# Kernel tuning notes

Measured on AMD Instinct MI355X. Metric: run time of the kernel, lower is better.

Reference implementation:

```python
import jax, jax.numpy as jnp
import numpy as np

N, E, D = 20000, 320000, 512


def _gat(x, W, a_src, a_dst, bias, src, dst, n, heads, ch):
    # PyG GATConv (eval mode, add_self_loops already applied via src/dst)
    h = (x @ W).reshape(n, heads, ch)              # [n, H, C]
    es = (h * a_src).sum(-1)                       # [n, H]
    ed = (h * a_dst).sum(-1)                       # [n, H]
    e = jax.nn.leaky_relu(es[src] + ed[dst], 0.2)  # [E, H]
    # edge-softmax grouped by destination node
    m = jax.ops.segment_max(e, dst, num_segments=n)
    ex = jnp.exp(e - m[dst])
    z = jax.ops.segment_sum(ex, dst, num_segments=n)
    alpha = ex / (z[dst] + 1e-16)                  # [E, H]
    out = jax.ops.segment_sum(h[src] * alpha[:, :, None], dst, num_segments=n)
    return out.reshape(n, heads * ch) + bias


def _ln(x, g, b):
    mu = x.mean(-1, keepdims=True)
    v = ((x - mu) ** 2).mean(-1, keepdims=True)
    return (x - mu) * jax.lax.rsqrt(v + 1e-5) * g + b


def setup_inputs() -> dict:
    key = jax.random.key(0)
    ks = jax.random.split(key, 24)
    p = lambda k, shape: jax.random.normal(k, shape, dtype=jnp.float32) * 0.05
    inp = {
        'x': jax.random.normal(ks[0], (N, D), dtype=jnp.float32),
        'edge_index': jax.random.randint(ks[1], (2, E), 0, N, dtype=jnp.int32),
        # GAT layer 1: 512 -> 8 heads x 128
        'w1': p(ks[2], (D, 1024)), 'as1': p(ks[3], (8, 128)), 'ad1': p(ks[4], (8, 128)), 'b1': jnp.zeros((1024,), jnp.float32),
        'g1': jnp.ones((1024,), jnp.float32), 'be1': jnp.zeros((1024,), jnp.float32),
        # GAT layer 2: 1024 -> 4 heads x 64
        'w2': p(ks[5], (1024, 256)), 'as2': p(ks[6], (4, 64)), 'ad2': p(ks[7], (4, 64)), 'b2': jnp.zeros((256,), jnp.float32),
        'g2': jnp.ones((256,), jnp.float32), 'be2': jnp.zeros((256,), jnp.float32),
        # GAT layer 3: 256 -> 2 heads x 32
        'w3': p(ks[8], (256, 64)), 'as3': p(ks[9], (2, 32)), 'ad3': p(ks[10], (2, 32)), 'b3': jnp.zeros((64,), jnp.float32),
        'g3': jnp.ones((64,), jnp.float32), 'be3': jnp.zeros((64,), jnp.float32),
        # anomaly scorer MLP
        'sw1': p(ks[11], (64, 64)), 'sb1': jnp.zeros((64,), jnp.float32),
        'sg1': jnp.ones((64,), jnp.float32), 'sbe1': jnp.zeros((64,), jnp.float32),
        'sw2': p(ks[12], (64, 32)), 'sb2': jnp.zeros((32,), jnp.float32),
        'sg2': jnp.ones((32,), jnp.float32), 'sbe2': jnp.zeros((32,), jnp.float32),
        'sw3': p(ks[13], (32, 1)), 'sb3': jnp.zeros((1,), jnp.float32),
    }
    return inp


def reference(x, edge_index, w1, as1, ad1, b1, g1, be1,
              w2, as2, ad2, b2, g2, be2,
              w3, as3, ad3, b3, g3, be3,
              sw1, sb1, sg1, sbe1, sw2, sb2, sg2, sbe2, sw3, sb3):
    loops = jnp.arange(N, dtype=edge_index.dtype)
    src = jnp.concatenate([edge_index[0], loops])  # add self-loops (PyG default)
    dst = jnp.concatenate([edge_index[1], loops])

    h1 = jax.nn.relu(_gat(x, w1, as1, ad1, b1, src, dst, N, 8, 128))
    h1 = _ln(h1, g1, be1)
    h2 = jax.nn.relu(_gat(h1, w2, as2, ad2, b2, src, dst, N, 4, 64))
    h2 = _ln(h2, g2, be2)
    h2 = h2 + h1[:, :256]
    h3 = jax.nn.relu(_gat(h2, w3, as3, ad3, b3, src, dst, N, 2, 32))
    h3 = _ln(h3, g3, be3)
    h3 = h3 + h2[:, :64]

    s = jax.nn.relu(h3 @ sw1 + sb1)
    s = _ln(s, sg1, sbe1)
    s = jax.nn.relu(s @ sw2 + sb2)
    s = _ln(s, sg2, sbe2)
    return jax.nn.sigmoid(s @ sw3 + sb3)  # [N, 1]
```

## Files before the change

### kernel.cpp

```cpp
#include <hip/hip_runtime.h>
#include <hip/hip_bf16.h>
#include <hip/hip_fp16.h>
#include <cstdint>

#define NN 20000
#define EE 320000
#define ETOT (EE + NN)

using f32x4 = __attribute__((ext_vector_type(4))) float;
using f16x8 = __attribute__((ext_vector_type(8))) _Float16;
typedef unsigned short ushortT;

__global__ void hist_kernel(const int* __restrict__ ei, int* __restrict__ deg) {
  int i = blockIdx.x * 256 + threadIdx.x;
  if (i >= ETOT) return;
  int d = (i < EE) ? ei[EE + i] : (i - EE);
  atomicAdd(&deg[d], 1);
}

__global__ __launch_bounds__(1024) void scan_kernel(const int* __restrict__ deg,
                                                    int* __restrict__ row_ptr,
                                                    int* __restrict__ cursor) {
  __shared__ int partial[1024];
  const int t = threadIdx.x;
  constexpr int PER = (NN + 1023) / 1024;
  const int base = t * PER;
  int vals[PER];
  int local = 0;
  #pragma unroll
  for (int j = 0; j < PER; ++j) {
    int i = base + j;
    int v = (i < NN) ? deg[i] : 0;
    vals[j] = v; local += v;
  }
  partial[t] = local;
  __syncthreads();
  for (int off = 1; off < 1024; off <<= 1) {
    int x = (t >= off) ? partial[t - off] : 0;
    __syncthreads();
    partial[t] += x;
    __syncthreads();
  }
  int prefix = partial[t] - local;
  #pragma unroll
  for (int j = 0; j < PER; ++j) {
    int i = base + j;
    if (i < NN) { row_ptr[i] = prefix; cursor[i] = prefix; }
    prefix += vals[j];
  }
  if (t == 1023) row_ptr[NN] = prefix;
}

__global__ void scatter_kernel(const int* __restrict__ ei, int* __restrict__ cursor,
                               int* __restrict__ csr_src) {
  int i = blockIdx.x * 256 + threadIdx.x;
  if (i >= ETOT) return;
  int s, d;
  if (i < EE) { s = ei[i]; d = ei[EE + i]; } else { s = d = i - EE; }
  int pos = atomicAdd(&cursor[d], 1);
  csr_src[pos] = s;
}

__global__ void half_mat(const float* __restrict__ a, __half* __restrict__ o, int n) {
  int i = blockIdx.x * 256 + threadIdx.x;
  if (i >= n) return;
  o[i] = __float2half(a[i]);
}

__global__ void tsplit_f16(const float* __restrict__ w, ushortT* __restrict__ hi,
                           ushortT* __restrict__ lo, int K, int M) {
  int i = blockIdx.x * 256 + threadIdx.x;
  if (i >= K * M) return;
  int k = i / M, c = i - k * M;
  float v = w[i];
  __half h = __float2half(v);
  __half l = __float2half(v - __half2float(h));
  size_t o = (size_t)c * K + k;
  hi[o] = __half_as_ushort(h);
  lo[o] = __half_as_ushort(l);
}

__device__ __forceinline__ void gload16(const void* g, void* l) {
  __builtin_amdgcn_global_load_lds((const __attribute__((address_space(1))) void*)g,
                                   (__attribute__((address_space(3))) void*)l, 16, 0, 0);
}

template<int BM, int BN, int FM, int FN, int CHEAD>
__global__ __launch_bounds__(256) void gemm_f16(
    const __half* __restrict__ A,
    const ushortT* __restrict__ Bhi, const ushortT* __restrict__ Blo,
    __half* __restrict__ C, int M, int Ncols, int K,
    const float* __restrict__ asrc, const float* __restrict__ adst,
    float* __restrict__ es_g, float* __restrict__ ed_g, int H)
{
  constexpr int BK = 32;
  __shared__ ushortT lds[(BM + 2 * BN) * BK];
  ushortT* sA  = lds;
  ushortT* sBh = sA + BM * BK;
  ushortT* sBl = sBh + BN * BK;

  const int tid  = threadIdx.x;
  const int lane = tid & 63;
  const int wid  = tid >> 6;
  const int wm   = (wid >> 1) * (FM * 16);
  const int wn   = (wid & 1) * (FN * 16);
  const int row0 = blockIdx.x * BM;
  const int col0 = blockIdx.y * BN;
  const int r    = lane & 15;
  const int kg   = lane >> 4;

  const ushortT* Au = (const ushortT*)A;
  f32x4 acc[FM][FN] = {};

  for (int k0 = 0; k0 < K; k0 += BK) {
    #pragma unroll
    for (int i = tid; i < BM * 4; i += 256) {
      int row = i >> 2, slot = i & 3;
      int gs = slot ^ (row & 3);
      int grow = row0 + row; if (grow > M - 1) grow = M - 1;
      gload16(Au + (size_t)grow * K + k0 + gs * 8, sA + row * BK + slot * 8);
    }
    #pragma unroll
    for (int i = tid; i < BN * 4; i += 256) {
      int row = i >> 2, slot = i & 3;
      int gs = slot ^ (row & 3);
      size_t go = (size_t)(col0 + row) * K + k0 + gs * 8;
      gload16(Bhi + go, sBh + row * BK + slot * 8);
      gload16(Blo + go, sBl + row * BK + slot * 8);
    }
    __syncthreads();

    const int ks = (kg ^ (r & 3)) * 8;
    f16x8 a[FM], bh[FN], bl[FN];
    #pragma unroll
    for (int mi = 0; mi < FM; ++mi)
      a[mi] = *(const f16x8*)(sA + (wm + mi * 16 + r) * BK + ks);
    #pragma unroll
    for (int ni = 0; ni < FN; ++ni) {
      int off = (wn + ni * 16 + r) * BK + ks;
      bh[ni] = *(const f16x8*)(sBh + off);
      bl[ni] = *(const f16x8*)(sBl + off);
    }
    #pragma unroll
    for (int mi = 0; mi < FM; ++mi)
      #pragma unroll
      for (int ni = 0; ni < FN; ++ni) {
        acc[mi][ni] = __builtin_amdgcn_mfma_f32_16x16x32_f16(a[mi], bh[ni], acc[mi][ni], 0, 0, 0);
        acc[mi][ni] = __builtin_amdgcn_mfma_f32_16x16x32_f16(a[mi], bl[ni], acc[mi][ni], 0, 0, 0);
      }
    __syncthreads();
  }

  #pragma unroll
  for (int mi = 0; mi < FM; ++mi) {
    int rb = row0 + wm + mi * 16 + (lane >> 4) * 4;
    #pragma unroll
    for (int ni = 0; ni < FN; ++ni) {
      int cc = col0 + wn + ni * 16 + (lane & 15);
      #pragma unroll
      for (int j = 0; j < 4; ++j) {
        int rr = rb + j;
        if (rr < M) C[(size_t)rr * Ncols + cc] = __float2half(acc[mi][ni][j]);
      }
    }
  }

  constexpr bool DIRECT = (CHEAD == FN * 16);
  float av[FN], dv[FN];
  #pragma unroll
  for (int ni = 0; ni < FN; ++ni) {
    int cc = col0 + wn + ni * 16 + (lane & 15);
    av[ni] = asrc[cc];
    dv[ni] = adst[cc];
  }
  float ps[FM][4], pd[FM][4];
  #pragma unroll
  for (int mi = 0; mi < FM; ++mi)
    #pragma unroll
    for (int j = 0; j < 4; ++j) {
      float s = 0.f, d = 0.f;
      #pragma unroll
      for (int ni = 0; ni < FN; ++ni) {
        float v = acc[mi][ni][j];
        s += v * av[ni];
        d += v * dv[ni];
      }
      #pragma unroll
      for (int off = 8; off; off >>= 1) {
        s += __shfl_xor(s, off);
        d += __shfl_xor(d, off);
      }
      ps[mi][j] = s; pd[mi][j] = d;
    }
  const int head = (col0 + wn) / CHEAD;
  if constexpr (DIRECT) {
    if ((lane & 15) == 0) {
      #pragma unroll
      for (int mi = 0; mi < FM; ++mi)
        #pragma unroll
        for (int j = 0; j < 4; ++j) {
          int rr = row0 + wm + mi * 16 + (lane >> 4) * 4 + j;
          if (rr < M) { es_g[rr * H + head] = ps[mi][j]; ed_g[rr * H + head] = pd[mi][j]; }
        }
    }
  } else {
    float* l_es = (float*)lds;
    float* l_ed = l_es + BM;
    if ((wid & 1) == 0 && (lane & 15) == 0) {
      #pragma unroll
      for (int mi = 0; mi < FM; ++mi)
        #pragma unroll
        for (int j = 0; j < 4; ++j) {
          int rl = wm + mi * 16 + (lane >> 4) * 4 + j;
          l_es[rl] = ps[mi][j]; l_ed[rl] = pd[mi][j];
        }
    }
    __syncthreads();
    if ((wid & 1) == 1 && (lane & 15) == 0) {
      #pragma unroll
      for (int mi = 0; mi < FM; ++mi)
        #pragma unroll
        for (int j = 0; j < 4; ++j) {
          int rl = wm + mi * 16 + (lane >> 4) * 4 + j;
          int rr = row0 + rl;
          if (rr < M) {
            es_g[rr * H + head] = ps[mi][j] + l_es[rl];
            ed_g[rr * H + head] = pd[mi][j] + l_ed[rl];
          }
        }
    }
  }
}

template<int VPT> struct GVec;
template<> struct GVec<16> { uint4 a, b; };
template<> struct GVec<4>  { uint2 a; };
template<> struct GVec<1>  { ushortT a; };

template<int VPT>
__device__ __forceinline__ GVec<VPT> gload(const __half* p) {
  GVec<VPT> v;
  if constexpr (VPT == 16) { v.a = *(const uint4*)p; v.b = *(const uint4*)(p + 8); }
  else if constexpr (VPT == 4) { v.a = *(const uint2*)p; }
  else { v.a = *(const ushortT*)p; }
  return v;
}

template<int VPT>
__device__ __forceinline__ void gfma(const GVec<VPT>& u, float w, float* acc) {
  if constexpr (VPT == 1) {
    __half hv;
    *(ushortT*)&hv = u.a;
    acc[0] += w * __half2float(hv);
  } else {
    const __half2* p = (const __half2*)&u;
    #pragma unroll
    for (int j = 0; j < VPT / 2; ++j) {
      float2 f = __half22float2(p[j]);
      acc[2 * j]     += w * f.x;
      acc[2 * j + 1] += w * f.y;
    }
  }
}

template<int H, int C, bool RES_IN, bool F16_OUT, bool SCORER, int WPB>
__global__ __launch_bounds__(WPB * 64, 2) void gat_agg_wave(
    const __half* __restrict__ h, const float* __restrict__ es_g, const float* __restrict__ ed_g,
    const int* __restrict__ row_ptr, const int* __restrict__ csr_src,
    const float* __restrict__ bias, const float* __restrict__ gamma, const float* __restrict__ beta,
    const __half* __restrict__ res_in, int res_stride, __half* __restrict__ out_h,
    const float* __restrict__ sw1, const float* __restrict__ sb1,
    const float* __restrict__ sg1, const float* __restrict__ sbe1,
    const float* __restrict__ sw2, const float* __restrict__ sb2,
    const float* __restrict__ sg2, const float* __restrict__ sbe2,
    const float* __restrict__ sw3, const float* __restrict__ sb3,
    float* __restrict__ out)
{
  constexpr int HC   = H * C;
  constexpr int VPT  = HC / 64;
  constexpr int CH   = 32;
  constexpr int BB   = (VPT == 16) ? 4 : 8;
  constexpr int LOGH = (H == 8) ? 3 : ((H == 4) ? 2 : 1);
  constexpr int EPR  = 64 >> LOGH;
  constexpr int ROUNDS = CH / EPR;

  const int wave = threadIdx.x >> 6;
  const int lane = threadIdx.x & 63;
  const int n    = blockIdx.x * WPB + wave;
  const int c0   = lane * VPT;
  const int myh  = c0 / C;
  const int wh   = lane & (H - 1);

  __shared__ float w_lds[WPB][(CH * H < 64) ? 64 : CH * H];
  float* wl = w_lds[wave];

  const int p0 = row_ptr[n];
  const int p1 = row_ptr[n + 1];
  const float edw = ed_g[n * H + wh];

  float acc[VPT];
  #pragma unroll
  for (int j = 0; j < VPT; ++j) acc[j] = 0.f;
  float z = 0.f;

  for (int base = p0; base < p1; base += CH) {
    const int m = min(CH, p1 - base);
    int sv = n;
    if (lane < CH) {
      int idx = base + lane;
      if (idx < p1) sv = csr_src[idx];
    }
    #pragma unroll
    for (int r = 0; r < ROUNDS; ++r) {
      int e = (lane >> LOGH) + r * EPR;
      int s = __shfl(sv, e);
      float w = 0.f;
      if (base + e < p1) {
        float ev = es_g[s * H + wh] + edw;
        ev = (ev >= 0.f) ? ev : 0.2f * ev;
        w = __expf(ev);
      }
      wl[e * H + wh] = w;
    }

    const int nb = m / BB;
    GVec<VPT> uA[BB], uB[BB];
    float wA[BB], wB[BB];

    auto LOADB = [&](int b, GVec<VPT> (&u)[BB], float (&w)[BB]) {
      #pragma unroll
      for (int k = 0; k < BB; ++k) {
        int e = b * BB + k;
        int s = __shfl(sv, e);
        w[k] = wl[e * H + myh];
        u[k] = gload<VPT>(h + (size_t)s * HC + c0);
      }
    };
    auto FMAB = [&](GVec<VPT> (&u)[BB], float (&w)[BB]) {
      #pragma unroll
      for (int k = 0; k < BB; ++k) {
        z += w[k];
        gfma<VPT>(u[k], w[k], acc);
      }
    };

    if (nb > 0) LOADB(0, uA, wA);
    #pragma unroll
    for (int bb = 0; bb < CH / BB; bb += 2) {
      if (bb < nb) {
        if (bb + 1 < nb) LOADB(bb + 1, uB, wB);
        FMAB(uA, wA);
      }
      if (bb + 1 < nb) {
        if (bb + 2 < nb) LOADB(bb + 2, uA, wA);
        FMAB(uB, wB);
      }
    }
    for (int e = nb * BB; e < m; ++e) {
      int s = __shfl(sv, e);
      float w = wl[e * H + myh];
      z += w;
      GVec<VPT> u = gload<VPT>(h + (size_t)s * HC + c0);
      gfma<VPT>(u, w, acc);
    }
  }

  float inv = 1.f / (z + 1e-16f);
  float ov[VPT];
  float psum = 0.f, psq = 0.f;
  #pragma unroll
  for (int j = 0; j < VPT; ++j) {
    float x = fmaxf(acc[j] * inv + bias[c0 + j], 0.f);
    ov[j] = x; psum += x; psq += x * x;
  }
  #pragma unroll
  for (int o = 32; o > 0; o >>= 1) {
    psum += __shfl_xor(psum, o);
    psq  += __shfl_xor(psq, o);
  }
  float mu  = psum / (float)HC;
  float var = psq / (float)HC - mu * mu;
  float rs  = rsqrtf(var + 1e-5f);

  ushortT hb[VPT > 1 ? VPT : 2];
  #pragma unroll
  for (int j = 0; j < VPT; ++j) {
    int c = c0 + j;
    float o = (ov[j] - mu) * rs * gamma[c] + beta[c];
    if constexpr (RES_IN) o += __half2float(res_in[(size_t)n * res_stride + c]);
    ov[j] = o;
    if constexpr (F16_OUT) hb[j] = __half_as_ushort(__float2half(o));
  }
  if constexpr (F16_OUT) {
    ushortT* po = (ushortT*)out_h + (size_t)n * HC + c0;
    if constexpr (VPT == 16) {
      *(uint4*)po       = *(uint4*)&hb[0];
      *(uint4*)(po + 8) = *(uint4*)&hb[8];
    } else if constexpr (VPT == 4) {
      *(uint2*)po = *(uint2*)&hb[0];
    } else {
      *po = hb[0];
    }
  }

  if constexpr (SCORER) {
    wl[lane] = ov[0];
    float s1 = sb1[lane];
    #pragma unroll 16
    for (int k = 0; k < 64; ++k) s1 += wl[k] * sw1[k * 64 + lane];
    s1 = fmaxf(s1, 0.f);
    float su = s1, sq = s1 * s1;
    #pragma unroll
    for (int o = 32; o > 0; o >>= 1) { su += __shfl_xor(su, o); sq += __shfl_xor(sq, o); }
    float mu1 = su * (1.f / 64.f), var1 = sq * (1.f / 64.f) - mu1 * mu1;
    float v1 = (s1 - mu1) * rsqrtf(var1 + 1e-5f) * sg1[lane] + sbe1[lane];
    wl[lane] = v1;
    float o2 = 0.f;
    if (lane < 32) {
      o2 = sb2[lane];
      #pragma unroll 16
      for (int k = 0; k < 64; ++k) o2 += wl[k] * sw2[k * 32 + lane];
      o2 = fmaxf(o2, 0.f);
    }
    float su2 = o2, sq2 = o2 * o2;
    #pragma unroll
    for (int o = 16; o > 0; o >>= 1) { su2 += __shfl_xor(su2, o); sq2 += __shfl_xor(sq2, o); }
    float p = 0.f;
    if (lane < 32) {
      float mu2 = su2 * (1.f / 32.f), var2 = sq2 * (1.f / 32.f) - mu2 * mu2;
      float v2 = (o2 - mu2) * rsqrtf(var2 + 1e-5f) * sg2[lane] + sbe2[lane];
      p = v2 * sw3[lane];
    }
    #pragma unroll
    for (int o = 16; o > 0; o >>= 1) p += __shfl_xor(p, o);
    if (lane == 0) out[n] = 1.f / (1.f + expf(-(p + sb3[0])));
  }
}

extern "C" void kernel_launch(void* const* d_in, const int* in_sizes, int n_in,
                              void* d_out, int out_size, void* d_ws, size_t ws_size,
                              hipStream_t stream)
{
  const float* x    = (const float*)d_in[0];
  const int*   ei   = (const int*)d_in[1];
  const float* w1   = (const float*)d_in[2];
  const float* as1  = (const float*)d_in[3];
  const float* ad1  = (const float*)d_in[4];
  const float* b1   = (const float*)d_in[5];
  const float* g1v  = (const float*)d_in[6];
  const float* be1  = (const float*)d_in[7];
  const float* w2   = (const float*)d_in[8];
  const float* as2  = (const float*)d_in[9];
  const float* ad2  = (const float*)d_in[10];
  const float* b2   = (const float*)d_in[11];
  const float* g2v  = (const float*)d_in[12];
  const float* be2  = (const float*)d_in[13];
  const float* w3   = (const float*)d_in[14];
  const float* as3  = (const float*)d_in[15];
  const float* ad3  = (const float*)d_in[16];
  const float* b3   = (const float*)d_in[17];
  const float* g3v  = (const float*)d_in[18];
  const float* be3  = (const float*)d_in[19];
  const float* sw1  = (const float*)d_in[20];
  const float* sb1  = (const float*)d_in[21];
  const float* sg1  = (const float*)d_in[22];
  const float* sbe1 = (const float*)d_in[23];
  const float* sw2  = (const float*)d_in[24];
  const float* sb2  = (const float*)d_in[25];
  const float* sg2  = (const float*)d_in[26];
  const float* sbe2 = (const float*)d_in[27];
  const float* sw3  = (const float*)d_in[28];
  const float* sb3  = (const float*)d_in[29];
  float* out = (float*)d_out;

  char* ws = (char*)d_ws;
  size_t off = 0;
  auto alloc = [&](size_t bytes) -> void* {
    off = (off + 255) & ~(size_t)255;
    void* p = ws + off;
    off += bytes;
    return p;
  };

  __half*  h_gemm  = (__half*)alloc((size_t)NN * 1024 * 2);
  __half*  h1_f16  = (__half*)alloc((size_t)NN * 1024 * 2);
  __half*  h2_f16  = (__half*)alloc((size_t)NN * 256 * 2);
  __half*  x16     = (__half*)alloc((size_t)NN * 512 * 2);
  ushortT* w1t_hi  = (ushortT*)alloc((size_t)512 * 1024 * 2);
  ushortT* w1t_lo  = (ushortT*)alloc((size_t)512 * 1024 * 2);
  ushortT* w2t_hi  = (ushortT*)alloc((size_t)1024 * 256 * 2);
  ushortT* w2t_lo  = (ushortT*)alloc((size_t)1024 * 256 * 2);
  ushortT* w3t_hi  = (ushortT*)alloc((size_t)256 * 64 * 2);
  ushortT* w3t_lo  = (ushortT*)alloc((size_t)256 * 64 * 2);
  float*   es_buf  = (float*)alloc((size_t)NN * 8 * 4);
  float*   ed_buf  = (float*)alloc((size_t)NN * 8 * 4);
  int*     deg     = (int*)alloc((size_t)NN * 4);
  int*     row_ptr = (int*)alloc((size_t)(NN + 1) * 4);
  int*     cursor  = (int*)alloc((size_t)NN * 4);
  int*     csr_src = (int*)alloc((size_t)ETOT * 4);
  (void)ws_size; (void)in_sizes; (void)n_in; (void)out_size;

  hipMemsetAsync(deg, 0, (size_t)NN * 4, stream);
  hist_kernel<<<(ETOT + 255) / 256, 256, 0, stream>>>(ei, deg);
  scan_kernel<<<1, 1024, 0, stream>>>(deg, row_ptr, cursor);
  scatter_kernel<<<(ETOT + 255) / 256, 256, 0, stream>>>(ei, cursor, csr_src);

  half_mat<<<(NN * 512 + 255) / 256, 256, 0, stream>>>(x, x16, NN * 512);
  tsplit_f16<<<(512 * 1024 + 255) / 256, 256, 0, stream>>>(w1, w1t_hi, w1t_lo, 512, 1024);
  tsplit_f16<<<(1024 * 256 + 255) / 256, 256, 0, stream>>>(w2, w2t_hi, w2t_lo, 1024, 256);
  tsplit_f16<<<(256 * 64 + 255) / 256, 256, 0, stream>>>(w3, w3t_hi, w3t_lo, 256, 64);

  const int MB = (NN + 127) / 128;

  gemm_f16<128, 128, 4, 4, 128><<<dim3(MB, 1024 / 128), 256, 0, stream>>>(
      x16, w1t_hi, w1t_lo, h_gemm, NN, 1024, 512, as1, ad1, es_buf, ed_buf, 8);
  gat_agg_wave<8, 128, false, true, false, 4><<<NN / 4, 256, 0, stream>>>(
      h_gemm, es_buf, ed_buf, row_ptr, csr_src, b1, g1v, be1,
      nullptr, 0, h1_f16,
      nullptr, nullptr, nullptr, nullptr, nullptr, nullptr, nullptr, nullptr, nullptr, nullptr, nullptr);

  gemm_f16<128, 128, 4, 4, 64><<<dim3(MB, 256 / 128), 256, 0, stream>>>(
      h1_f16, w2t_hi, w2t_lo, h_gemm, NN, 256, 1024, as2, ad2, es_buf, ed_buf, 4);
  gat_agg_wave<4, 64, true, true, false, 4><<<NN / 4, 256, 0, stream>>>(
      h_gemm, es_buf, ed_buf, row_ptr, csr_src, b2, g2v, be2,
      h1_f16, 1024, h2_f16,
      nullptr, nullptr, nullptr, nullptr, nullptr, nullptr, nullptr, nullptr, nullptr, nullptr, nullptr);

  gemm_f16<128, 64, 4, 2, 32><<<dim3(MB, 1), 256, 0, stream>>>(
      h2_f16, w3t_hi, w3t_lo, h_gemm, NN, 64, 256, as3, ad3, es_buf, ed_buf, 2);
  gat_agg_wave<2, 32, true, false, true, 4><<<NN / 4, 256, 0, stream>>>(
      h_gemm, es_buf, ed_buf, row_ptr, csr_src, b3, g3v, be3,
      h2_f16, 256, nullptr,
      sw1, sb1, sg1, sbe1, sw2, sb2, sg2, sbe2, sw3, sb3, out);
}
```

Baseline: 382.8 us.

## Double-buffer GEMM LDS stages and vectorize GAT aggregation index/weight loads

The GEMM now double-buffers its LDS tiles. It issues the next K-tile's global-to-LDS loads before computing on the current one, using explicit vmcnt waits and raw barriers in place of __syncthreads, so load latency overlaps the MFMA work. In the aggregation kernel, source indices are staged in LDS instead of being broadcast with per-edge shuffles. Attention weights are stored head-major with padding so four weights and four indices can be read as float4/int4. The batch size BB is fixed at 4 for every layer. This doubles GEMM LDS use, which may reduce occupancy, and relies on the hand-coded vmcnt counts matching the number of issued loads.

```diff
diff --git a/kernel.cpp b/kernel.cpp
--- a/kernel.cpp
+++ b/kernel.cpp
@@ -85,6 +85,13 @@
                                    (__attribute__((address_space(3))) void*)l, 16, 0, 0);
 }
 
+template<int N> __device__ __forceinline__ void wait_vm() {
+  if constexpr (N == 0) asm volatile("s_waitcnt vmcnt(0)" ::: "memory");
+  else if constexpr (N == 4) asm volatile("s_waitcnt vmcnt(4)" ::: "memory");
+  else if constexpr (N == 6) asm volatile("s_waitcnt vmcnt(6)" ::: "memory");
+  else static_assert(N == 0 || N == 4 || N == 6, "unsupported vmcnt");
+}
+
 template<int BM, int BN, int FM, int FN, int CHEAD>
 __global__ __launch_bounds__(256) void gemm_f16(
     const __half* __restrict__ A,
@@ -93,11 +100,10 @@
     const float* __restrict__ asrc, const float* __restrict__ adst,
     float* __restrict__ es_g, float* __restrict__ ed_g, int H)
 {
-  constexpr int BK = 32;
-  __shared__ ushortT lds[(BM + 2 * BN) * BK];
-  ushortT* sA  = lds;
-  ushortT* sBh = sA + BM * BK;
-  ushortT* sBl = sBh + BN * BK;
+  constexpr int BK   = 32;
+  constexpr int HALF = (BM + 2 * BN) * BK;
+  constexpr int NL   = (BM * 4 + BN * 8) / 256;
+  __shared__ ushortT lds[2 * HALF];
 
   const int tid  = threadIdx.x;
   const int lane = tid & 63;
@@ -110,9 +116,11 @@
   const int kg   = lane >> 4;
 
   const ushortT* Au = (const ushortT*)A;
-  f32x4 acc[FM][FN] = {};
-
-  for (int k0 = 0; k0 < K; k0 += BK) {
+
+  auto STAGE = [&](int buf, int k0) {
+    ushortT* sA  = lds + buf * HALF;
+    ushortT* sBh = sA + BM * BK;
+    ushortT* sBl = sBh + BN * BK;
     #pragma unroll
     for (int i = tid; i < BM * 4; i += 256) {
       int row = i >> 2, slot = i & 3;
@@ -128,8 +136,21 @@
       gload16(Bhi + go, sBh + row * BK + slot * 8);
       gload16(Blo + go, sBl + row * BK + slot * 8);
     }
-    __syncthreads();
-
+  };
+
+  f32x4 acc[FM][FN] = {};
+  const int nt = K / BK;
+
+  STAGE(0, 0);
+  for (int t = 0; t < nt; ++t) {
+    if (t + 1 < nt) { STAGE((t + 1) & 1, (t + 1) * BK); wait_vm<NL>(); }
+    else            { wait_vm<0>(); }
+    __builtin_amdgcn_s_barrier();
+    __builtin_amdgcn_sched_barrier(0);
+
+    const ushortT* sA  = lds + (t & 1) * HALF;
+    const ushortT* sBh = sA + BM * BK;
+    const ushortT* sBl = sBh + BN * BK;
     const int ks = (kg ^ (r & 3)) * 8;
     f16x8 a[FM], bh[FN], bl[FN];
     #pragma unroll
@@ -148,7 +169,8 @@
         acc[mi][ni] = __builtin_amdgcn_mfma_f32_16x16x32_f16(a[mi], bh[ni], acc[mi][ni], 0, 0, 0);
         acc[mi][ni] = __builtin_amdgcn_mfma_f32_16x16x32_f16(a[mi], bl[ni], acc[mi][ni], 0, 0, 0);
       }
-    __syncthreads();
+    __builtin_amdgcn_sched_barrier(0);
+    __builtin_amdgcn_s_barrier();
   }
 
   #pragma unroll
@@ -206,6 +228,7 @@
   } else {
     float* l_es = (float*)lds;
     float* l_ed = l_es + BM;
+    __syncthreads();
     if ((wid & 1) == 0 && (lane & 15) == 0) {
       #pragma unroll
       for (int mi = 0; mi < FM; ++mi)
@@ -279,10 +302,11 @@
   constexpr int HC   = H * C;
   constexpr int VPT  = HC / 64;
   constexpr int CH   = 32;
-  constexpr int BB   = (VPT == 16) ? 4 : 8;
+  constexpr int BB   = 4;
   constexpr int LOGH = (H == 8) ? 3 : ((H == 4) ? 2 : 1);
   constexpr int EPR  = 64 >> LOGH;
   constexpr int ROUNDS = CH / EPR;
+  constexpr int WST  = CH + 4;
 
   const int wave = threadIdx.x >> 6;
   const int lane = threadIdx.x & 63;
@@ -291,7 +315,9 @@
   const int myh  = c0 / C;
   const int wh   = lane & (H - 1);
 
-  __shared__ float w_lds[WPB][(CH * H < 64) ? 64 : CH * H];
+  __shared__ int   s_lds[WPB][CH];
+  __shared__ float w_lds[WPB][H * WST];
+  int*   sl = s_lds[wave];
   float* wl = w_lds[wave];
 
   const int p0 = row_ptr[n];
@@ -305,43 +331,38 @@
 
   for (int base = p0; base < p1; base += CH) {
     const int m = min(CH, p1 - base);
-    int sv = n;
-    if (lane < CH) {
-      int idx = base + lane;
-      if (idx < p1) sv = csr_src[idx];
-    }
-    #pragma unroll
-    for (int r = 0; r < ROUNDS; ++r) {
-      int e = (lane >> LOGH) + r * EPR;
-      int s = __shfl(sv, e);
+    if (lane < CH) sl[lane] = (base + lane < p1) ? csr_src[base + lane] : n;
+    #pragma unroll
+    for (int rr = 0; rr < ROUNDS; ++rr) {
+      int e = (lane >> LOGH) + rr * EPR;
+      int s = sl[e];
       float w = 0.f;
       if (base + e < p1) {
         float ev = es_g[s * H + wh] + edw;
         ev = (ev >= 0.f) ? ev : 0.2f * ev;
         w = __expf(ev);
       }
-      wl[e * H + wh] = w;
+      wl[wh * WST + e] = w;
     }
 
     const int nb = m / BB;
     GVec<VPT> uA[BB], uB[BB];
-    float wA[BB], wB[BB];
-
-    auto LOADB = [&](int b, GVec<VPT> (&u)[BB], float (&w)[BB]) {
-      #pragma unroll
-      for (int k = 0; k < BB; ++k) {
-        int e = b * BB + k;
-        int s = __shfl(sv, e);
-        w[k] = wl[e * H + myh];
-        u[k] = gload<VPT>(h + (size_t)s * HC + c0);
-      }
+    float4 wA, wB;
+
+    auto LOADB = [&](int b, GVec<VPT> (&u)[BB], float4& w4) {
+      int4 s4 = *(const int4*)&sl[b * BB];
+      w4 = *(const float4*)&wl[myh * WST + b * BB];
+      u[0] = gload<VPT>(h + (size_t)s4.x * HC + c0);
+      u[1] = gload<VPT>(h + (size_t)s4.y * HC + c0);
+      u[2] = gload<VPT>(h + (size_t)s4.z * HC + c0);
+      u[3] = gload<VPT>(h + (size_t)s4.w * HC + c0);
     };
-    auto FMAB = [&](GVec<VPT> (&u)[BB], float (&w)[BB]) {
-      #pragma unroll
-      for (int k = 0; k < BB; ++k) {
-        z += w[k];
-        gfma<VPT>(u[k], w[k], acc);
-      }
+    auto FMAB = [&](GVec<VPT> (&u)[BB], float4& w4) {
+      z += w4.x + w4.y + w4.z + w4.w;
+      gfma<VPT>(u[0], w4.x, acc);
+      gfma<VPT>(u[1], w4.y, acc);
+      gfma<VPT>(u[2], w4.z, acc);
+      gfma<VPT>(u[3], w4.w, acc);
     };
 
     if (nb > 0) LOADB(0, uA, wA);
@@ -357,8 +378,8 @@
       }
     }
     for (int e = nb * BB; e < m; ++e) {
-      int s = __shfl(sv, e);
-      float w = wl[e * H + myh];
+      int s = sl[e];
+      float w = wl[myh * WST + e];
       z += w;
       GVec<VPT> u = gload<VPT>(h + (size_t)s * HC + c0);
       gfma<VPT>(u, w, acc);
```

Measured after the change: 362.6 us. 5.3% less time.
